# Kernel tuning notes

Measured on AMD Instinct MI355X. Metric: run time of the kernel, lower is better.

## Reference

```python
import jax, jax.numpy as jnp
import numpy as np

N, E, D = 20000, 320000, 256
H, C = 8, 32  # heads, per-head channels (out_channels // heads)


def setup_inputs() -> dict:
    key = jax.random.key(0)
    ks = jax.random.split(key, 12)
    s = 1.0 / np.sqrt(D)
    return {
        "x": jax.random.normal(ks[0], (N, D), jnp.float32),
        "edge_index": jax.random.randint(ks[1], (2, E), 0, N, jnp.int64),
        "edge_attr": jax.random.normal(ks[2], (E, D), jnp.float32),
        "Wq": jax.random.normal(ks[3], (D, H * C), jnp.float32) * s,
        "bq": jnp.zeros((H * C,), jnp.float32),
        "Wk": jax.random.normal(ks[4], (D, H * C), jnp.float32) * s,
        "bk": jnp.zeros((H * C,), jnp.float32),
        "Wv": jax.random.normal(ks[5], (D, H * C), jnp.float32) * s,
        "bv": jnp.zeros((H * C,), jnp.float32),
        "We": jax.random.normal(ks[6], (D, H * C), jnp.float32) * s,  # lin_edge, no bias
        "Ws": jax.random.normal(ks[7], (D, H * C), jnp.float32) * s,  # lin_skip (root weight)
        "bs": jnp.zeros((H * C,), jnp.float32),
    }


def reference(x, edge_index, edge_attr, Wq, bq, Wk, bk, Wv, bv, We, Ws, bs):
    n = x.shape[0]
    src, dst = edge_index[0], edge_index[1]  # j (source), i (target)
    q = (x @ Wq + bq).reshape(n, H, C)
    k = (x @ Wk + bk).reshape(n, H, C)
    v = (x @ Wv + bv).reshape(n, H, C)
    e = (edge_attr @ We).reshape(-1, H, C)  # (E, H, C)

    kj = k[src] + e                      # key of source node + edge embedding
    alpha = jnp.einsum('ehc,ehc->eh', q[dst], kj) / jnp.sqrt(jnp.float32(C))
    # numerically-stable segment softmax over destination neighborhoods
    amax = jax.ops.segment_max(alpha, dst, num_segments=n)      # (N, H)
    ea = jnp.exp(alpha - amax[dst])                             # (E, H)
    denom = jax.ops.segment_sum(ea, dst, num_segments=n)        # (N, H)
    alpha = ea / (denom[dst] + 1e-16)

    msg = (v[src] + e) * alpha[:, :, None]                      # (E, H, C)
    out = jax.ops.segment_sum(msg, dst, num_segments=n)         # (N, H, C)
    out = out.reshape(n, H * C) + (x @ Ws + bs)                 # concat heads + skip
    return out
```

## Files before the change

kernel.cpp:

```cpp
#include <hip/hip_runtime.h>
#include <hip/hip_fp16.h>

#define N_NODES 20000
#define N_EDGES 320000
#define DIM 256

typedef _Float16 f16;
typedef unsigned int u32;
typedef f16 f16x8 __attribute__((ext_vector_type(8)));
typedef f16 f16x4 __attribute__((ext_vector_type(4)));
typedef float f32x4 __attribute__((ext_vector_type(4)));

#define GLL16(gsrc, ldst) __builtin_amdgcn_global_load_lds( \
    (const u32 __attribute__((address_space(1)))*)(gsrc),   \
    (u32 __attribute__((address_space(3)))*)(ldst), 16, 0, 0)

__global__ void prep_all(const float* __restrict__ Wq, const float* __restrict__ Wk,
                         const float* __restrict__ Wv, const float* __restrict__ Ws,
                         const float* __restrict__ We,
                         const float* __restrict__ bq, const float* __restrict__ bk,
                         const float* __restrict__ bv, const float* __restrict__ bs,
                         f16* __restrict__ wtbase, f16* __restrict__ wef16,
                         float* __restrict__ biasAll, int* __restrict__ deg) {
    if (blockIdx.x < 1280) {
        int gid = blockIdx.x * 256 + threadIdx.x;
        int w = gid >> 16;
        int idx = gid & 65535;
        int k = idx >> 8, n = idx & 255;
        const float* W = (w == 0) ? Wq : (w == 1) ? Wk : (w == 2) ? Wv : (w == 3) ? Ws : We;
        wtbase[w * 65536 + n * 256 + k] = (f16)W[k * 256 + n];
    } else if (blockIdx.x < 1536) {
        int idx = (blockIdx.x - 1280) * 256 + threadIdx.x;
        wef16[idx] = (f16)We[idx];
    } else if (blockIdx.x < 1540) {
        int i = (blockIdx.x - 1536) * 256 + threadIdx.x;
        int y = i >> 8, col = i & 255;
        const float* b = (y == 0) ? bq : (y == 1) ? bk : (y == 2) ? bv : bs;
        biasAll[i] = b[col];
    } else {
        int i = (blockIdx.x - 1540) * 256 + threadIdx.x;
        if (i < N_NODES) deg[i] = 0;
    }
}

__global__ __launch_bounds__(512, 4) void gemm_qkvs(
    const float* __restrict__ A, const f16* __restrict__ WTbase,
    const float* __restrict__ biasAll,
    f16* __restrict__ outF16, float* __restrict__ outF32)
{
    __shared__ __align__(16) char lds[65536];
    const int tid = threadIdx.x;
    const int wave = tid >> 6, lane = tid & 63;
    const int l16 = lane & 15, lg = lane >> 4;
    const int y = blockIdx.y;
    const int outSel = y >> 1, colHalf = y & 1;
    const f16* __restrict__ WT = WTbase + outSel * 65536 + colHalf * 128 * 256;
    const int rowBase = blockIdx.x * 128 + wave * 16;

    const int slot = rowBase + l16;
    const int arow = (slot < N_NODES) ? slot : N_NODES - 1;
    const float* ap = A + (size_t)arow * DIM;
    f32x4 lo[8], hi[8];
#pragma unroll
    for (int ks = 0; ks < 8; ++ks) {
        lo[ks] = *(const f32x4*)(ap + ks * 32 + lg * 8);
        hi[ks] = *(const f32x4*)(ap + ks * 32 + lg * 8 + 4);
    }
    {
        const int p = lane & 31;
#pragma unroll
        for (int r = 0; r < 8; ++r) {
            const int nrel = wave * 16 + r * 2 + (lane >> 5);
            const f16* src = WT + nrel * 256 + (p ^ (nrel & 31)) * 8;
            GLL16(src, &lds[(wave * 16 + r * 2) * 512]);
        }
    }
    f16x8 afr[8];
#pragma unroll
    for (int ks = 0; ks < 8; ++ks) {
#pragma unroll
        for (int j = 0; j < 4; ++j) {
            afr[ks][j]     = (f16)lo[ks][j];
            afr[ks][4 + j] = (f16)hi[ks][j];
        }
    }
    f32x4 acc[8];
#pragma unroll
    for (int c = 0; c < 8; ++c) acc[c] = (f32x4){0.f, 0.f, 0.f, 0.f};

    __syncthreads();

#pragma unroll
    for (int ks = 0; ks < 8; ++ks) {
#pragma unroll
        for (int ct = 0; ct < 8; ++ct) {
            const int nrel = ct * 16 + l16;
            f16x8 b = *(const f16x8*)(lds + nrel * 512 + (((ks * 4 + lg) ^ (nrel & 31)) * 16));
            acc[ct] = __builtin_amdgcn_mfma_f32_16x16x32_f16(afr[ks], b, acc[ct], 0, 0, 0);
        }
    }
#pragma unroll
    for (int ct = 0; ct < 8; ++ct) {
        const int col = colHalf * 128 + ct * 16 + l16;
        const float bv = biasAll[outSel * 256 + col];
#pragma unroll
        for (int i = 0; i < 4; ++i) {
            const int row = rowBase + lg * 4 + i;
            if (row < N_NODES) {
                const float val = acc[ct][i] + bv;
                if (outSel < 3)
                    (outF16 + (size_t)outSel * N_NODES * 256)[(size_t)row * 256 + col] = (f16)val;
                else
                    outF32[(size_t)row * 256 + col] = val;
            }
        }
    }
}

__global__ __launch_bounds__(256, 4) void gemm_g(
    const f16* __restrict__ qf, const f16* __restrict__ wef16, f16* __restrict__ G)
{
    const int tid = threadIdx.x;
    const int wave = tid >> 6, lane = tid & 63;
    const int l16 = lane & 15, lg = lane >> 4;
    const int h = blockIdx.y;
    const int rowBase = blockIdx.x * 64 + wave * 16;

    int arow = rowBase + l16;
    if (arow >= N_NODES) arow = N_NODES - 1;
    f16x8 a = *(const f16x8*)(qf + (size_t)arow * 256 + h * 32 + lg * 8);

    f32x4 acc[16];
#pragma unroll
    for (int c = 0; c < 16; ++c) acc[c] = (f32x4){0.f, 0.f, 0.f, 0.f};
#pragma unroll
    for (int ct = 0; ct < 16; ++ct) {
        f16x8 b = *(const f16x8*)(wef16 + (size_t)(ct * 16 + l16) * 256 + h * 32 + lg * 8);
        acc[ct] = __builtin_amdgcn_mfma_f32_16x16x32_f16(a, b, acc[ct], 0, 0, 0);
    }
#pragma unroll
    for (int ct = 0; ct < 16; ++ct) {
        const int d = ct * 16 + l16;
#pragma unroll
        for (int i = 0; i < 4; ++i) {
            const int row = rowBase + lg * 4 + i;
            if (row < N_NODES)
                G[(size_t)row * 2048 + h * 256 + d] = (f16)acc[ct][i];
        }
    }
}

__global__ void count_deg(const int* __restrict__ dst, int* __restrict__ deg) {
    int e = blockIdx.x * blockDim.x + threadIdx.x;
    if (e < N_EDGES) atomicAdd(&deg[dst[e]], 1);
}

__global__ __launch_bounds__(1024) void scan_deg(const int* __restrict__ deg,
                                                 int* __restrict__ rowptr,
                                                 int* __restrict__ cursor) {
    __shared__ int part[1024];
    const int t = threadIdx.x;
    const int CH = (N_NODES + 1023) / 1024;
    const int base = t * CH;
    int s = 0;
    for (int i = 0; i < CH; ++i) { int n = base + i; if (n < N_NODES) s += deg[n]; }
    part[t] = s;
    __syncthreads();
    for (int off = 1; off < 1024; off <<= 1) {
        int v = (t >= off) ? part[t - off] : 0;
        __syncthreads();
        part[t] += v;
        __syncthreads();
    }
    int run = (t == 0) ? 0 : part[t - 1];
    for (int i = 0; i < CH; ++i) {
        int n = base + i;
        if (n < N_NODES) { int dn = deg[n]; rowptr[n] = run; cursor[n] = run; run += dn; }
    }
    if (t == 1023) rowptr[N_NODES] = part[1023];
}

__global__ void scatter_edges(const int* __restrict__ src, const int* __restrict__ dst,
                              int* __restrict__ cursor,
                              int* __restrict__ eids, int* __restrict__ srcs) {
    int e = blockIdx.x * blockDim.x + threadIdx.x;
    if (e < N_EDGES) {
        int p = atomicAdd(&cursor[dst[e]], 1);
        eids[p] = e;
        srcs[p] = src[e];
    }
}

__global__ __launch_bounds__(256) void aggregate3(
    const f16* __restrict__ qf, const f16* __restrict__ kf, const f16* __restrict__ vf,
    f16* __restrict__ G, const float* __restrict__ ea,
    const int* __restrict__ eids, const int* __restrict__ srcs,
    const int* __restrict__ rowptr, float* __restrict__ out)
{
    const int wave = threadIdx.x >> 6;
    const int lane = threadIdx.x & 63;
    const int node = blockIdx.x * 4 + wave;
    if (node >= N_NODES) return;
    const int h = lane >> 3, j = lane & 7;
    const int c0 = lane * 4;

    f32x4 qv;
    {
        f16x4 qh = *(const f16x4*)(qf + (size_t)node * 256 + c0);
        qv = (f32x4){(float)qh[0], (float)qh[1], (float)qh[2], (float)qh[3]};
    }
    f32x4 ga[8];
#pragma unroll
    for (int m = 0; m < 8; ++m) {
        f16x4 gh = *(const f16x4*)(G + (size_t)node * 2048 + h * 256 + m * 32 + j * 4);
        ga[m] = (f32x4){(float)gh[0], (float)gh[1], (float)gh[2], (float)gh[3]};
    }

    f32x4 z[8];
#pragma unroll
    for (int m = 0; m < 8; ++m) z[m] = (f32x4){0.f, 0.f, 0.f, 0.f};
    f32x4 va = (f32x4){0.f, 0.f, 0.f, 0.f};
    float den = 0.f;
    const int beg = rowptr[node], end = rowptr[node + 1];

    int eid = 0, src = 0;
    if (beg < end) { eid = eids[beg]; src = srcs[beg]; }
    for (int idx = beg; idx < end; ++idx) {
        const int eidN = (idx + 1 < end) ? eids[idx + 1] : 0;
        const int srcN = (idx + 1 < end) ? srcs[idx + 1] : 0;
        const float* ep = ea + (size_t)eid * 256 + j * 4;
        f32x4 e0 = *(const f32x4*)(ep + 0 * 32);
        f32x4 e1 = *(const f32x4*)(ep + 1 * 32);
        f32x4 e2 = *(const f32x4*)(ep + 2 * 32);
        f32x4 e3 = *(const f32x4*)(ep + 3 * 32);
        f32x4 e4 = *(const f32x4*)(ep + 4 * 32);
        f32x4 e5 = *(const f32x4*)(ep + 5 * 32);
        f32x4 e6 = *(const f32x4*)(ep + 6 * 32);
        f32x4 e7 = *(const f32x4*)(ep + 7 * 32);
        f16x4 kh = *(const f16x4*)(kf + (size_t)src * 256 + c0);
        f16x4 vh = *(const f16x4*)(vf + (size_t)src * 256 + c0);

        float p = 0.f;
#define DOT4(ev, m_) p += (ev)[0]*ga[m_][0] + (ev)[1]*ga[m_][1] + (ev)[2]*ga[m_][2] + (ev)[3]*ga[m_][3]
        DOT4(e0, 0); DOT4(e1, 1); DOT4(e2, 2); DOT4(e3, 3);
        DOT4(e4, 4); DOT4(e5, 5); DOT4(e6, 6); DOT4(e7, 7);
#undef DOT4
        p += qv[0]*(float)kh[0] + qv[1]*(float)kh[1] + qv[2]*(float)kh[2] + qv[3]*(float)kh[3];
        p += __shfl_xor(p, 1);
        p += __shfl_xor(p, 2);
        p += __shfl_xor(p, 4);
        const float al = __expf(p * 0.1767766952966369f);
        den += al;
        va[0] += al * (float)vh[0]; va[1] += al * (float)vh[1];
        va[2] += al * (float)vh[2]; va[3] += al * (float)vh[3];
#define ZACC(ev, m_) { z[m_][0] += al*(ev)[0]; z[m_][1] += al*(ev)[1]; z[m_][2] += al*(ev)[2]; z[m_][3] += al*(ev)[3]; }
        ZACC(e0, 0); ZACC(e1, 1); ZACC(e2, 2); ZACC(e3, 3);
        ZACC(e4, 4); ZACC(e5, 5); ZACC(e6, 6); ZACC(e7, 7);
#undef ZACC
        eid = eidN; src = srcN;
    }

    const float inv = 1.0f / (den + 1e-16f);
    const size_t ob = (size_t)node * 256 + c0;
    f32x4 o = *(f32x4*)(out + ob);
    o[0] += va[0] * inv; o[1] += va[1] * inv; o[2] += va[2] * inv; o[3] += va[3] * inv;
    *(f32x4*)(out + ob) = o;
#pragma unroll
    for (int m = 0; m < 8; ++m) {
        f16x4 zh;
        zh[0] = (f16)(z[m][0] * inv); zh[1] = (f16)(z[m][1] * inv);
        zh[2] = (f16)(z[m][2] * inv); zh[3] = (f16)(z[m][3] * inv);
        *(f16x4*)(G + (size_t)node * 2048 + h * 256 + m * 32 + j * 4) = zh;
    }
}

__global__ __launch_bounds__(512, 4) void gemm_z2(
    const f16* __restrict__ zf, const f16* __restrict__ WTe, float* __restrict__ out)
{
    const int tid = threadIdx.x;
    const int wave = tid >> 6, lane = tid & 63;
    const int l16 = lane & 15, lg = lane >> 4;
    const int h = blockIdx.y;
    const int rowBase = blockIdx.x * 128 + wave * 16;

    int arow = rowBase + l16;
    if (arow >= N_NODES) arow = N_NODES - 1;
    const f16* ap = zf + (size_t)arow * 2048 + h * 256 + lg * 8;

    f32x4 acc[2];
    acc[0] = (f32x4){0.f, 0.f, 0.f, 0.f};
    acc[1] = (f32x4){0.f, 0.f, 0.f, 0.f};
#pragma unroll
    for (int ks = 0; ks < 8; ++ks) {
        f16x8 a = *(const f16x8*)(ap + ks * 32);
#pragma unroll
        for (int ct = 0; ct < 2; ++ct) {
            f16x8 b = *(const f16x8*)(WTe + (size_t)(h * 32 + ct * 16 + l16) * 256 + ks * 32 + lg * 8);
            acc[ct] = __builtin_amdgcn_mfma_f32_16x16x32_f16(a, b, acc[ct], 0, 0, 0);
        }
    }
#pragma unroll
    for (int ct = 0; ct < 2; ++ct) {
        const int col = h * 32 + ct * 16 + l16;
#pragma unroll
        for (int i = 0; i < 4; ++i) {
            const int row = rowBase + lg * 4 + i;
            if (row < N_NODES)
                out[(size_t)row * 256 + col] += acc[ct][i];
        }
    }
}

extern "C" void kernel_launch(void* const* d_in, const int* in_sizes, int n_in,
                              void* d_out, int out_size, void* d_ws, size_t ws_size,
                              hipStream_t stream) {
    const float* x   = (const float*)d_in[0];
    const int*   ei  = (const int*)d_in[1];
    const float* ea  = (const float*)d_in[2];
    const float* Wq  = (const float*)d_in[3];
    const float* bq  = (const float*)d_in[4];
    const float* Wk  = (const float*)d_in[5];
    const float* bk  = (const float*)d_in[6];
    const float* Wv  = (const float*)d_in[7];
    const float* bv  = (const float*)d_in[8];
    const float* We  = (const float*)d_in[9];
    const float* Ws  = (const float*)d_in[10];
    const float* bs  = (const float*)d_in[11];
    float* out = (float*)d_out;

    const int* srcArr = ei;
    const int* dstArr = ei + N_EDGES;

    char* w = (char*)d_ws;
    size_t off = 0;
    f16* wtbase = (f16*)(w + off); off += 5 * 65536 * 2;
    f16* wef16  = (f16*)(w + off); off += 65536 * 2;
    f16* qf = (f16*)(w + off); off += (size_t)N_NODES * 256 * 2;
    f16* kf = (f16*)(w + off); off += (size_t)N_NODES * 256 * 2;
    f16* vf = (f16*)(w + off); off += (size_t)N_NODES * 256 * 2;
    f16* G  = (f16*)(w + off); off += (size_t)N_NODES * 2048 * 2;
    int* deg    = (int*)(w + off); off += 80016;
    int* rowptr = (int*)(w + off); off += 80016;
    int* cursor = (int*)(w + off); off += 80016;
    int* eids   = (int*)(w + off); off += (size_t)N_EDGES * 4;
    int* srcs   = (int*)(w + off); off += (size_t)N_EDGES * 4;
    float* biasAll = (float*)(w + off); off += 4 * 256 * 4;
    (void)ws_size; (void)n_in; (void)in_sizes; (void)out_size;

    prep_all<<<1540 + (N_NODES + 255) / 256, 256, 0, stream>>>(
        Wq, Wk, Wv, Ws, We, bq, bk, bv, bs, wtbase, wef16, biasAll, deg);

    count_deg<<<(N_EDGES + 255) / 256, 256, 0, stream>>>(dstArr, deg);
    scan_deg<<<1, 1024, 0, stream>>>(deg, rowptr, cursor);
    scatter_edges<<<(N_EDGES + 255) / 256, 256, 0, stream>>>(srcArr, dstArr, cursor, eids, srcs);

    dim3 gnode((N_NODES + 127) / 128, 8);
    gemm_qkvs<<<gnode, 512, 0, stream>>>(x, wtbase, biasAll, qf, out);

    dim3 gg((N_NODES + 63) / 64, 8);
    gemm_g<<<gg, 256, 0, stream>>>(qf, wef16, G);

    aggregate3<<<(N_NODES + 3) / 4, 256, 0, stream>>>(
        qf, kf, vf, G, ea, eids, srcs, rowptr, out);

    dim3 gz((N_NODES + 127) / 128, 8);
    gemm_z2<<<gz, 512, 0, stream>>>(G, wtbase + 4 * 65536, out);
}
```

Before: 449.7 us.

## Double-buffer edge loads in aggregation and pack edge id/src into int2

The aggregation loop now software-pipelines two edges: it issues the gathers of edge attributes and k/v rows for the next two edges while computing the current ones, so more memory requests are in flight per wave. Edge id and source are stored together as int2, so one 8-byte load replaces two separate index loads. The dot-product reduction is rebalanced into a tree, and launch bounds ask for 3 blocks per CU. The cost is roughly double the register footprint for the edge buffers, which may limit occupancy, and the tail handling adds code complexity.

```diff
diff --git a/kernel.cpp b/kernel.cpp
--- a/kernel.cpp
+++ b/kernel.cpp
@@ -181,21 +181,19 @@
 }
 
 __global__ void scatter_edges(const int* __restrict__ src, const int* __restrict__ dst,
-                              int* __restrict__ cursor,
-                              int* __restrict__ eids, int* __restrict__ srcs) {
+                              int* __restrict__ cursor, int2* __restrict__ es) {
     int e = blockIdx.x * blockDim.x + threadIdx.x;
     if (e < N_EDGES) {
         int p = atomicAdd(&cursor[dst[e]], 1);
-        eids[p] = e;
-        srcs[p] = src[e];
-    }
-}
-
-__global__ __launch_bounds__(256) void aggregate3(
+        es[p] = make_int2(e, src[e]);
+    }
+}
+
+__global__ __launch_bounds__(256, 3) void aggregate4(
     const f16* __restrict__ qf, const f16* __restrict__ kf, const f16* __restrict__ vf,
     f16* __restrict__ G, const float* __restrict__ ea,
-    const int* __restrict__ eids, const int* __restrict__ srcs,
-    const int* __restrict__ rowptr, float* __restrict__ out)
+    const int2* __restrict__ es, const int* __restrict__ rowptr,
+    float* __restrict__ out)
 {
     const int wave = threadIdx.x >> 6;
     const int lane = threadIdx.x & 63;
@@ -222,43 +220,66 @@
     f32x4 va = (f32x4){0.f, 0.f, 0.f, 0.f};
     float den = 0.f;
     const int beg = rowptr[node], end = rowptr[node + 1];
-
-    int eid = 0, src = 0;
-    if (beg < end) { eid = eids[beg]; src = srcs[beg]; }
-    for (int idx = beg; idx < end; ++idx) {
-        const int eidN = (idx + 1 < end) ? eids[idx + 1] : 0;
-        const int srcN = (idx + 1 < end) ? srcs[idx + 1] : 0;
-        const float* ep = ea + (size_t)eid * 256 + j * 4;
-        f32x4 e0 = *(const f32x4*)(ep + 0 * 32);
-        f32x4 e1 = *(const f32x4*)(ep + 1 * 32);
-        f32x4 e2 = *(const f32x4*)(ep + 2 * 32);
-        f32x4 e3 = *(const f32x4*)(ep + 3 * 32);
-        f32x4 e4 = *(const f32x4*)(ep + 4 * 32);
-        f32x4 e5 = *(const f32x4*)(ep + 5 * 32);
-        f32x4 e6 = *(const f32x4*)(ep + 6 * 32);
-        f32x4 e7 = *(const f32x4*)(ep + 7 * 32);
-        f16x4 kh = *(const f16x4*)(kf + (size_t)src * 256 + c0);
-        f16x4 vh = *(const f16x4*)(vf + (size_t)src * 256 + c0);
-
-        float p = 0.f;
-#define DOT4(ev, m_) p += (ev)[0]*ga[m_][0] + (ev)[1]*ga[m_][1] + (ev)[2]*ga[m_][2] + (ev)[3]*ga[m_][3]
-        DOT4(e0, 0); DOT4(e1, 1); DOT4(e2, 2); DOT4(e3, 3);
-        DOT4(e4, 4); DOT4(e5, 5); DOT4(e6, 6); DOT4(e7, 7);
-#undef DOT4
-        p += qv[0]*(float)kh[0] + qv[1]*(float)kh[1] + qv[2]*(float)kh[2] + qv[3]*(float)kh[3];
-        p += __shfl_xor(p, 1);
-        p += __shfl_xor(p, 2);
-        p += __shfl_xor(p, 4);
-        const float al = __expf(p * 0.1767766952966369f);
-        den += al;
-        va[0] += al * (float)vh[0]; va[1] += al * (float)vh[1];
-        va[2] += al * (float)vh[2]; va[3] += al * (float)vh[3];
-#define ZACC(ev, m_) { z[m_][0] += al*(ev)[0]; z[m_][1] += al*(ev)[1]; z[m_][2] += al*(ev)[2]; z[m_][3] += al*(ev)[3]; }
-        ZACC(e0, 0); ZACC(e1, 1); ZACC(e2, 2); ZACC(e3, 3);
-        ZACC(e4, 4); ZACC(e5, 5); ZACC(e6, 6); ZACC(e7, 7);
-#undef ZACC
-        eid = eidN; src = srcN;
-    }
+    const int n = end - beg;
+
+    f32x4 eA[8], eB[8];
+    f16x4 kA, vA, kB, vB;
+
+#define ISSUE(E_, K_, V_, slot_) do {                                          \
+        const int2 _es = es[slot_];                                            \
+        const float* _ep = ea + (size_t)_es.x * 256 + j * 4;                   \
+        _Pragma("unroll")                                                      \
+        for (int _m = 0; _m < 8; ++_m) E_[_m] = *(const f32x4*)(_ep + _m * 32);\
+        K_ = *(const f16x4*)(kf + (size_t)_es.y * 256 + c0);                   \
+        V_ = *(const f16x4*)(vf + (size_t)_es.y * 256 + c0);                   \
+    } while (0)
+
+#define COMPUTE(E_, K_, V_) do {                                               \
+        float _dm[8];                                                          \
+        _Pragma("unroll")                                                      \
+        for (int _m = 0; _m < 8; ++_m)                                         \
+            _dm[_m] = E_[_m][0]*ga[_m][0] + E_[_m][1]*ga[_m][1]                \
+                    + E_[_m][2]*ga[_m][2] + E_[_m][3]*ga[_m][3];               \
+        float _p = ((_dm[0]+_dm[1]) + (_dm[2]+_dm[3]))                         \
+                 + ((_dm[4]+_dm[5]) + (_dm[6]+_dm[7]));                        \
+        _p += qv[0]*(float)K_[0] + qv[1]*(float)K_[1]                          \
+            + qv[2]*(float)K_[2] + qv[3]*(float)K_[3];                         \
+        _p += __shfl_xor(_p, 1);                                               \
+        _p += __shfl_xor(_p, 2);                                               \
+        _p += __shfl_xor(_p, 4);                                               \
+        const float _al = __expf(_p * 0.1767766952966369f);                    \
+        den += _al;                                                            \
+        va[0] += _al * (float)V_[0]; va[1] += _al * (float)V_[1];              \
+        va[2] += _al * (float)V_[2]; va[3] += _al * (float)V_[3];              \
+        _Pragma("unroll")                                                      \
+        for (int _m = 0; _m < 8; ++_m) {                                       \
+            z[_m][0] += _al * E_[_m][0]; z[_m][1] += _al * E_[_m][1];          \
+            z[_m][2] += _al * E_[_m][2]; z[_m][3] += _al * E_[_m][3];          \
+        }                                                                      \
+    } while (0)
+
+    if (n >= 2) {
+        ISSUE(eA, kA, vA, beg);
+        ISSUE(eB, kB, vB, beg + 1);
+        int i = beg;
+        for (; i + 3 < end; i += 2) {
+            COMPUTE(eA, kA, vA); ISSUE(eA, kA, vA, i + 2);
+            COMPUTE(eB, kB, vB); ISSUE(eB, kB, vB, i + 3);
+        }
+        if (i + 2 < end) {
+            COMPUTE(eA, kA, vA); ISSUE(eA, kA, vA, i + 2);
+            COMPUTE(eB, kB, vB);
+            COMPUTE(eA, kA, vA);
+        } else {
+            COMPUTE(eA, kA, vA);
+            COMPUTE(eB, kB, vB);
+        }
+    } else if (n == 1) {
+        ISSUE(eA, kA, vA, beg);
+        COMPUTE(eA, kA, vA);
+    }
+#undef ISSUE
+#undef COMPUTE
 
     const float inv = 1.0f / (den + 1e-16f);
     const size_t ob = (size_t)node * 256 + c0;
@@ -342,8 +363,7 @@
     int* deg    = (int*)(w + off); off += 80016;
     int* rowptr = (int*)(w + off); off += 80016;
     int* cursor = (int*)(w + off); off += 80016;
-    int* eids   = (int*)(w + off); off += (size_t)N_EDGES * 4;
-    int* srcs   = (int*)(w + off); off += (size_t)N_EDGES * 4;
+    int2* es    = (int2*)(w + off); off += (size_t)N_EDGES * 8;
     float* biasAll = (float*)(w + off); off += 4 * 256 * 4;
     (void)ws_size; (void)n_in; (void)in_sizes; (void)out_size;
 
@@ -352,7 +372,7 @@
 
     count_deg<<<(N_EDGES + 255) / 256, 256, 0, stream>>>(dstArr, deg);
     scan_deg<<<1, 1024, 0, stream>>>(deg, rowptr, cursor);
-    scatter_edges<<<(N_EDGES + 255) / 256, 256, 0, stream>>>(srcArr, dstArr, cursor, eids, srcs);
+    scatter_edges<<<(N_EDGES + 255) / 256, 256, 0, stream>>>(srcArr, dstArr, cursor, es);
 
     dim3 gnode((N_NODES + 127) / 128, 8);
     gemm_qkvs<<<gnode, 512, 0, stream>>>(x, wtbase, biasAll, qf, out);
@@ -360,8 +380,8 @@
     dim3 gg((N_NODES + 63) / 64, 8);
     gemm_g<<<gg, 256, 0, stream>>>(qf, wef16, G);
 
-    aggregate3<<<(N_NODES + 3) / 4, 256, 0, stream>>>(
-        qf, kf, vf, G, ea, eids, srcs, rowptr, out);
+    aggregate4<<<(N_NODES + 3) / 4, 256, 0, stream>>>(
+        qf, kf, vf, G, ea, es, rowptr, out);
 
     dim3 gz((N_NODES + 127) / 128, 8);
     gemm_z2<<<gz, 512, 0, stream>>>(G, wtbase + 4 * 65536, out);
```

Result: slower. 695.8 us (+54.7%).

## Split each node's edge loop across two waves and pack edge id/src pairs

Applied to the files above, without the earlier changes.

The aggregation kernel now gives each destination node two wavefronts, which take alternating edges and then merge partial softmax numerators, denominators and z accumulators through shared memory. This doubles the memory-level parallelism on the edge_attr gather, which is the dominant cost. Edge ids and sources are packed into a single int2 array so one load fetches both, and the per-edge dot product is reassociated into a tree to shorten the dependency chain. In exchange the kernel adds a shared-memory reduction, a block barrier and about 37KB of LDS per block, which may lower occupancy.

```diff
diff --git a/kernel.cpp b/kernel.cpp
--- a/kernel.cpp
+++ b/kernel.cpp
@@ -181,26 +181,25 @@
 }
 
 __global__ void scatter_edges(const int* __restrict__ src, const int* __restrict__ dst,
-                              int* __restrict__ cursor,
-                              int* __restrict__ eids, int* __restrict__ srcs) {
+                              int* __restrict__ cursor, int2* __restrict__ es) {
     int e = blockIdx.x * blockDim.x + threadIdx.x;
     if (e < N_EDGES) {
         int p = atomicAdd(&cursor[dst[e]], 1);
-        eids[p] = e;
-        srcs[p] = src[e];
-    }
-}
-
-__global__ __launch_bounds__(256) void aggregate3(
+        es[p] = make_int2(e, src[e]);
+    }
+}
+
+__global__ __launch_bounds__(256) void aggregate5(
     const f16* __restrict__ qf, const f16* __restrict__ kf, const f16* __restrict__ vf,
     f16* __restrict__ G, const float* __restrict__ ea,
-    const int* __restrict__ eids, const int* __restrict__ srcs,
-    const int* __restrict__ rowptr, float* __restrict__ out)
+    const int2* __restrict__ es, const int* __restrict__ rowptr,
+    float* __restrict__ out)
 {
+    __shared__ float red[4][64][37];
     const int wave = threadIdx.x >> 6;
     const int lane = threadIdx.x & 63;
-    const int node = blockIdx.x * 4 + wave;
-    if (node >= N_NODES) return;
+    const int sub  = wave & 1;
+    const int node = blockIdx.x * 2 + (wave >> 1);
     const int h = lane >> 3, j = lane & 7;
     const int c0 = lane * 4;
 
@@ -223,12 +222,12 @@
     float den = 0.f;
     const int beg = rowptr[node], end = rowptr[node + 1];
 
-    int eid = 0, src = 0;
-    if (beg < end) { eid = eids[beg]; src = srcs[beg]; }
-    for (int idx = beg; idx < end; ++idx) {
-        const int eidN = (idx + 1 < end) ? eids[idx + 1] : 0;
-        const int srcN = (idx + 1 < end) ? srcs[idx + 1] : 0;
-        const float* ep = ea + (size_t)eid * 256 + j * 4;
+    int idx = beg + sub;
+    int2 cur;
+    if (idx < end) cur = es[idx];
+    for (; idx < end; idx += 2) {
+        const int2 nxt = (idx + 2 < end) ? es[idx + 2] : make_int2(0, 0);
+        const float* ep = ea + (size_t)cur.x * 256 + j * 4;
         f32x4 e0 = *(const f32x4*)(ep + 0 * 32);
         f32x4 e1 = *(const f32x4*)(ep + 1 * 32);
         f32x4 e2 = *(const f32x4*)(ep + 2 * 32);
@@ -237,14 +236,18 @@
         f32x4 e5 = *(const f32x4*)(ep + 5 * 32);
         f32x4 e6 = *(const f32x4*)(ep + 6 * 32);
         f32x4 e7 = *(const f32x4*)(ep + 7 * 32);
-        f16x4 kh = *(const f16x4*)(kf + (size_t)src * 256 + c0);
-        f16x4 vh = *(const f16x4*)(vf + (size_t)src * 256 + c0);
-
-        float p = 0.f;
-#define DOT4(ev, m_) p += (ev)[0]*ga[m_][0] + (ev)[1]*ga[m_][1] + (ev)[2]*ga[m_][2] + (ev)[3]*ga[m_][3]
-        DOT4(e0, 0); DOT4(e1, 1); DOT4(e2, 2); DOT4(e3, 3);
-        DOT4(e4, 4); DOT4(e5, 5); DOT4(e6, 6); DOT4(e7, 7);
-#undef DOT4
+        f16x4 kh = *(const f16x4*)(kf + (size_t)cur.y * 256 + c0);
+        f16x4 vh = *(const f16x4*)(vf + (size_t)cur.y * 256 + c0);
+
+        float dm0 = e0[0]*ga[0][0] + e0[1]*ga[0][1] + e0[2]*ga[0][2] + e0[3]*ga[0][3];
+        float dm1 = e1[0]*ga[1][0] + e1[1]*ga[1][1] + e1[2]*ga[1][2] + e1[3]*ga[1][3];
+        float dm2 = e2[0]*ga[2][0] + e2[1]*ga[2][1] + e2[2]*ga[2][2] + e2[3]*ga[2][3];
+        float dm3 = e3[0]*ga[3][0] + e3[1]*ga[3][1] + e3[2]*ga[3][2] + e3[3]*ga[3][3];
+        float dm4 = e4[0]*ga[4][0] + e4[1]*ga[4][1] + e4[2]*ga[4][2] + e4[3]*ga[4][3];
+        float dm5 = e5[0]*ga[5][0] + e5[1]*ga[5][1] + e5[2]*ga[5][2] + e5[3]*ga[5][3];
+        float dm6 = e6[0]*ga[6][0] + e6[1]*ga[6][1] + e6[2]*ga[6][2] + e6[3]*ga[6][3];
+        float dm7 = e7[0]*ga[7][0] + e7[1]*ga[7][1] + e7[2]*ga[7][2] + e7[3]*ga[7][3];
+        float p = ((dm0 + dm1) + (dm2 + dm3)) + ((dm4 + dm5) + (dm6 + dm7));
         p += qv[0]*(float)kh[0] + qv[1]*(float)kh[1] + qv[2]*(float)kh[2] + qv[3]*(float)kh[3];
         p += __shfl_xor(p, 1);
         p += __shfl_xor(p, 2);
@@ -253,24 +256,47 @@
         den += al;
         va[0] += al * (float)vh[0]; va[1] += al * (float)vh[1];
         va[2] += al * (float)vh[2]; va[3] += al * (float)vh[3];
-#define ZACC(ev, m_) { z[m_][0] += al*(ev)[0]; z[m_][1] += al*(ev)[1]; z[m_][2] += al*(ev)[2]; z[m_][3] += al*(ev)[3]; }
-        ZACC(e0, 0); ZACC(e1, 1); ZACC(e2, 2); ZACC(e3, 3);
-        ZACC(e4, 4); ZACC(e5, 5); ZACC(e6, 6); ZACC(e7, 7);
-#undef ZACC
-        eid = eidN; src = srcN;
-    }
-
-    const float inv = 1.0f / (den + 1e-16f);
-    const size_t ob = (size_t)node * 256 + c0;
-    f32x4 o = *(f32x4*)(out + ob);
-    o[0] += va[0] * inv; o[1] += va[1] * inv; o[2] += va[2] * inv; o[3] += va[3] * inv;
-    *(f32x4*)(out + ob) = o;
-#pragma unroll
-    for (int m = 0; m < 8; ++m) {
-        f16x4 zh;
-        zh[0] = (f16)(z[m][0] * inv); zh[1] = (f16)(z[m][1] * inv);
-        zh[2] = (f16)(z[m][2] * inv); zh[3] = (f16)(z[m][3] * inv);
-        *(f16x4*)(G + (size_t)node * 2048 + h * 256 + m * 32 + j * 4) = zh;
+        z[0][0] += al*e0[0]; z[0][1] += al*e0[1]; z[0][2] += al*e0[2]; z[0][3] += al*e0[3];
+        z[1][0] += al*e1[0]; z[1][1] += al*e1[1]; z[1][2] += al*e1[2]; z[1][3] += al*e1[3];
+        z[2][0] += al*e2[0]; z[2][1] += al*e2[1]; z[2][2] += al*e2[2]; z[2][3] += al*e2[3];
+        z[3][0] += al*e3[0]; z[3][1] += al*e3[1]; z[3][2] += al*e3[2]; z[3][3] += al*e3[3];
+        z[4][0] += al*e4[0]; z[4][1] += al*e4[1]; z[4][2] += al*e4[2]; z[4][3] += al*e4[3];
+        z[5][0] += al*e5[0]; z[5][1] += al*e5[1]; z[5][2] += al*e5[2]; z[5][3] += al*e5[3];
+        z[6][0] += al*e6[0]; z[6][1] += al*e6[1]; z[6][2] += al*e6[2]; z[6][3] += al*e6[3];
+        z[7][0] += al*e7[0]; z[7][1] += al*e7[1]; z[7][2] += al*e7[2]; z[7][3] += al*e7[3];
+        cur = nxt;
+    }
+
+    {
+        float* rp = &red[wave][lane][0];
+#pragma unroll
+        for (int m = 0; m < 8; ++m) {
+            rp[m * 4 + 0] = z[m][0]; rp[m * 4 + 1] = z[m][1];
+            rp[m * 4 + 2] = z[m][2]; rp[m * 4 + 3] = z[m][3];
+        }
+        rp[32] = va[0]; rp[33] = va[1]; rp[34] = va[2]; rp[35] = va[3];
+        rp[36] = den;
+    }
+    __syncthreads();
+    if (sub == 0) {
+        const float* ra = &red[wave][lane][0];
+        const float* rb = &red[wave + 1][lane][0];
+        const float dsum = ra[36] + rb[36];
+        const float inv = 1.0f / (dsum + 1e-16f);
+        const size_t ob = (size_t)node * 256 + c0;
+        f32x4 o = *(f32x4*)(out + ob);
+        o[0] += (ra[32] + rb[32]) * inv; o[1] += (ra[33] + rb[33]) * inv;
+        o[2] += (ra[34] + rb[34]) * inv; o[3] += (ra[35] + rb[35]) * inv;
+        *(f32x4*)(out + ob) = o;
+#pragma unroll
+        for (int m = 0; m < 8; ++m) {
+            f16x4 zh;
+            zh[0] = (f16)((ra[m * 4 + 0] + rb[m * 4 + 0]) * inv);
+            zh[1] = (f16)((ra[m * 4 + 1] + rb[m * 4 + 1]) * inv);
+            zh[2] = (f16)((ra[m * 4 + 2] + rb[m * 4 + 2]) * inv);
+            zh[3] = (f16)((ra[m * 4 + 3] + rb[m * 4 + 3]) * inv);
+            *(f16x4*)(G + (size_t)node * 2048 + h * 256 + m * 32 + j * 4) = zh;
+        }
     }
 }
 
@@ -342,8 +368,7 @@
     int* deg    = (int*)(w + off); off += 80016;
     int* rowptr = (int*)(w + off); off += 80016;
     int* cursor = (int*)(w + off); off += 80016;
-    int* eids   = (int*)(w + off); off += (size_t)N_EDGES * 4;
-    int* srcs   = (int*)(w + off); off += (size_t)N_EDGES * 4;
+    int2* es    = (int2*)(w + off); off += (size_t)N_EDGES * 8;
     float* biasAll = (float*)(w + off); off += 4 * 256 * 4;
     (void)ws_size; (void)n_in; (void)in_sizes; (void)out_size;
 
@@ -352,7 +377,7 @@
 
     count_deg<<<(N_EDGES + 255) / 256, 256, 0, stream>>>(dstArr, deg);
     scan_deg<<<1, 1024, 0, stream>>>(deg, rowptr, cursor);
-    scatter_edges<<<(N_EDGES + 255) / 256, 256, 0, stream>>>(srcArr, dstArr, cursor, eids, srcs);
+    scatter_edges<<<(N_EDGES + 255) / 256, 256, 0, stream>>>(srcArr, dstArr, cursor, es);
 
     dim3 gnode((N_NODES + 127) / 128, 8);
     gemm_qkvs<<<gnode, 512, 0, stream>>>(x, wtbase, biasAll, qf, out);
@@ -360,8 +385,8 @@
     dim3 gg((N_NODES + 63) / 64, 8);
     gemm_g<<<gg, 256, 0, stream>>>(qf, wef16, G);
 
-    aggregate3<<<(N_NODES + 3) / 4, 256, 0, stream>>>(
-        qf, kf, vf, G, ea, eids, srcs, rowptr, out);
+    aggregate5<<<N_NODES / 2, 256, 0, stream>>>(
+        qf, kf, vf, G, ea, es, rowptr, out);
 
     dim3 gz((N_NODES + 127) / 128, 8);
     gemm_z2<<<gz, 512, 0, stream>>>(G, wtbase + 4 * 65536, out);
```

Measured after the change: 450.5 us. About the same (+0.2%).
